# Kernel optimization log

Hardware: AMD Instinct MI355X
Metric: run time of the kernel (lower is better)

Reference implementation:

```python
import jax, jax.numpy as jnp
import numpy as np

K_PRESERVE = 256
NUM_NEW = 1
UNITS = 768
HEAD_DIM = 64
N_HEADS = UNITS // HEAD_DIM
HID = 768


def setup_inputs() -> dict:
    key = jax.random.key(0)
    ks = jax.random.split(key, 12)
    B, H, L, D = 32, 12, 512, HID
    s = 0.02
    return {
        "hidden_states": jax.random.normal(ks[0], (B, L, D), jnp.float32),
        "attention_mask": jnp.zeros((B, 1, 1, L), jnp.float32),
        "self_attention_scores": jax.random.normal(ks[1], (B, H, L, L), jnp.float32),
        "Wq": jax.random.normal(ks[2], (D, UNITS), jnp.float32) * s,
        "bq": jnp.zeros((UNITS,), jnp.float32),
        "Wk": jax.random.normal(ks[3], (D, UNITS), jnp.float32) * s,
        "bk": jnp.zeros((UNITS,), jnp.float32),
        "Wv": jax.random.normal(ks[4], (D, UNITS), jnp.float32) * s,
        "bv": jnp.zeros((UNITS,), jnp.float32),
        "Wo": jax.random.normal(ks[5], (UNITS, D), jnp.float32) * s,
        "bo": jnp.zeros((D,), jnp.float32),
    }


def _forward(hidden_states, attention_mask, self_attention_scores,
             Wq, bq, Wk, bk, Wv, bv, Wo, bo):
    B, L, D = hidden_states.shape
    # K after reserving the new token slot
    K = max(min(K_PRESERVE, L) - NUM_NEW, 1)

    am = attention_mask.reshape(B, L)                      # additive mask as [B,L]
    amf = (am > -10.0).astype(jnp.float32)
    elem = amf[:, :, None] * amf[:, None, :]               # [B,L,L]
    scores = self_attention_scores * elem[:, None, :, :]   # [B,H,L,L]

    imp = scores.mean(axis=1).mean(axis=1)                 # [B,L]
    imp = imp.at[:, 0].set(jnp.inf)                        # always keep CLS
    _, idx = jax.lax.top_k(imp, K)                         # [B,K]
    idx = jnp.sort(idx, axis=-1)                           # boolean-mask gather keeps order

    preserved = jnp.take_along_axis(hidden_states, idx[:, :, None], axis=1)  # [B,K,D]
    preserved_mask = jnp.take_along_axis(am, idx, axis=1).reshape(B, 1, 1, K)

    # sentence vector = softmax(mask) @ hidden
    att = jax.nn.softmax(am, axis=-1)                      # [B,L]
    sentences = jnp.einsum('bl,bld->bd', att, hidden_states)[:, None, :]  # [B,1,D]
    key_pad = am < -10.0                                    # [B,L] True = masked

    # small cross-attention producing one new token
    q = (sentences @ Wq + bq).reshape(B, 1, N_HEADS, HEAD_DIM)
    k = (hidden_states @ Wk + bk).reshape(B, L, N_HEADS, HEAD_DIM)
    v = (hidden_states @ Wv + bv).reshape(B, L, N_HEADS, HEAD_DIM)
    logits = jnp.einsum('bqhd,blhd->bhql', q, k) / np.sqrt(HEAD_DIM).astype(np.float32)
    logits = jnp.where(key_pad[:, None, None, :], -jnp.inf, logits)
    w = jax.nn.softmax(logits, axis=-1)                    # [B,H,1,L]
    ctx = jnp.einsum('bhql,blhd->bqhd', w, v).reshape(B, 1, UNITS)
    new_token = ctx @ Wo + bo                              # [B,1,D]

    final_token = jnp.concatenate([preserved, new_token], axis=1)         # [B,K+1,D]
    new_mask = jnp.zeros((B, 1, 1, 1), jnp.float32)
    final_mask = jnp.concatenate([preserved_mask, new_mask], axis=-1)     # [B,1,1,K+1]
    tome_size = jnp.ones((B, K + 1, 1), jnp.float32)
    return final_token, final_mask, tome_size


def reference(hidden_states, attention_mask, self_attention_scores,
              Wq, bq, Wk, bk, Wv, bv, Wo, bo):
    return _forward(hidden_states, attention_mask, self_attention_scores,
                    Wq, bq, Wk, bk, Wv, bv, Wo, bo)
```

## Files before the change

### kernel.cpp

```cpp
#include <hip/hip_runtime.h>
#include <cstdint>
#include <cstddef>

#define B 32
#define H 12
#define L 512
#define D 768
#define KSEL 255

#define OFF_IMP   0
#define MEMSET_BYTES 65536
#define OFF_SENT  65536
#define OFF_Y     163840
#define OFF_ATT   1343488
#define OFF_Q     1409024
#define OFF_A     1507328
#define OFF_CB    2686976
#define OFF_LG    2688512
#define OFF_SEL   3474944
#define OFF_CTX   3507584

__global__ __launch_bounds__(128) void k_imp(const float* __restrict__ sas,
                                             const float* __restrict__ am,
                                             float* __restrict__ imp) {
  const int b = blockIdx.x, h = blockIdx.y, ch = blockIdx.z;
  const int t = threadIdx.x;
  const float* base = sas + (((size_t)(b * H + h)) * L + (size_t)ch * 128) * L;
  const float* amb = am + b * L + ch * 128;
  float a0 = 0, a1 = 0, a2 = 0, a3 = 0;
#pragma unroll 8
  for (int l = 0; l < 128; ++l) {
    const float m = (amb[l] > -10.0f) ? 1.0f : 0.0f;
    const float4 v = reinterpret_cast<const float4*>(base + (size_t)l * L)[t];
    a0 += m * v.x;
    a1 += m * v.y;
    a2 += m * v.z;
    a3 += m * v.w;
  }
  float* ip = imp + b * L + t * 4;
  atomicAdd(ip + 0, a0);
  atomicAdd(ip + 1, a1);
  atomicAdd(ip + 2, a2);
  atomicAdd(ip + 3, a3);
}

__global__ __launch_bounds__(512) void k_prep(const float* __restrict__ am,
                                              const float* __restrict__ imp,
                                              float* __restrict__ att,
                                              int* __restrict__ sel,
                                              float* __restrict__ out_mask,
                                              float* __restrict__ out_tome,
                                              float* __restrict__ sent) {
  const int b = blockIdx.x, l = threadIdx.x;
  __shared__ float r1[8], r2[8];
  __shared__ float v[512];
  __shared__ int sc[512];
  sent[b * D + l] = 0.0f;
  if (l < D - 512) sent[b * D + 512 + l] = 0.0f;
  const float aml = am[b * L + l];
  float m = aml;
#pragma unroll
  for (int o = 32; o; o >>= 1) m = fmaxf(m, __shfl_down(m, o));
  if ((l & 63) == 0) r1[l >> 6] = m;
  __syncthreads();
  if (l == 0) {
    float mm = r1[0];
    for (int i = 1; i < 8; ++i) mm = fmaxf(mm, r1[i]);
    r1[0] = mm;
  }
  __syncthreads();
  const float M = r1[0];
  const float e = expf(aml - M);
  float s = e;
#pragma unroll
  for (int o = 32; o; o >>= 1) s += __shfl_down(s, o);
  if ((l & 63) == 0) r2[l >> 6] = s;
  __syncthreads();
  if (l == 0) {
    float ss = 0.f;
    for (int i = 0; i < 8; ++i) ss += r2[i];
    r2[0] = ss;
  }
  __syncthreads();
  att[b * L + l] = e / r2[0];
  float val;
  if (l == 0)
    val = INFINITY;
  else
    val = (aml > -10.0f) ? imp[b * L + l] : 0.0f;
  v[l] = val;
  __syncthreads();
  int r = 0;
  for (int t = 0; t < 512; ++t) {
    const float vt = v[t];
    r += (vt > val) || (vt == val && t < l);
  }
  const int f = (r < KSEL) ? 1 : 0;
  sc[l] = f;
  __syncthreads();
  for (int off = 1; off < 512; off <<= 1) {
    const int add = (l >= off) ? sc[l - off] : 0;
    __syncthreads();
    sc[l] += add;
    __syncthreads();
  }
  if (f) {
    const int pos = sc[l] - 1;
    sel[b * KSEL + pos] = l;
    out_mask[b * 256 + pos] = aml;
  }
  if (l == 0) out_mask[b * 256 + 255] = 0.0f;
  if (l < 256) out_tome[b * 256 + l] = 1.0f;
}

__global__ __launch_bounds__(256) void k_gather(const float* __restrict__ hs,
                                                const int* __restrict__ sel,
                                                float* __restrict__ out_tok) {
  const int row = blockIdx.x * 4 + (threadIdx.x >> 6);
  const int lane = threadIdx.x & 63;
  const int b = row / KSEL, p = row % KSEL;
  const int j = sel[row];
  const float4* src = reinterpret_cast<const float4*>(hs + ((size_t)b * L + j) * D);
  float4* dst = reinterpret_cast<float4*>(out_tok + ((size_t)b * 256 + p) * D);
#pragma unroll
  for (int i = 0; i < 3; ++i) dst[lane + 64 * i] = src[lane + 64 * i];
}

__global__ __launch_bounds__(768) void k_sent(const float* __restrict__ hs,
                                              const float* __restrict__ att,
                                              float* __restrict__ sent) {
  const int b = blockIdx.x, c = blockIdx.y, t = threadIdx.x;
  __shared__ float a[64];
  if (t < 64) a[t] = att[b * L + c * 64 + t];
  __syncthreads();
  const float* h0 = hs + ((size_t)b * L + c * 64) * D;
  float acc = 0.f;
  for (int l = 0; l < 64; ++l) acc += a[l] * h0[(size_t)l * D + t];
  atomicAdd(&sent[b * D + t], acc);
}

__global__ __launch_bounds__(512) void k_q(const float* __restrict__ sent,
                                           const float* __restrict__ Wq,
                                           const float* __restrict__ bq,
                                           const float* __restrict__ bk,
                                           float* __restrict__ qg,
                                           float* __restrict__ cbg) {
  const int h = blockIdx.x;
  const int b = blockIdx.y * 8 + (threadIdx.x >> 6);
  const int ul = threadIdx.x & 63;
  const int u = h * 64 + ul;
  const float* sb = sent + b * D;
  float a0 = 0.f, a1 = 0.f, a2 = 0.f, a3 = 0.f;
#pragma unroll 4
  for (int d = 0; d < D; d += 4) {
    a0 += sb[d + 0] * Wq[(size_t)(d + 0) * D + u];
    a1 += sb[d + 1] * Wq[(size_t)(d + 1) * D + u];
    a2 += sb[d + 2] * Wq[(size_t)(d + 2) * D + u];
    a3 += sb[d + 3] * Wq[(size_t)(d + 3) * D + u];
  }
  const float acc = bq[u] + ((a0 + a1) + (a2 + a3));
  qg[b * D + u] = acc;
  float v = bk[u] * acc;
#pragma unroll
  for (int o = 32; o; o >>= 1) v += __shfl_down(v, o);
  if (ul == 0) cbg[b * H + h] = v;
}

__global__ __launch_bounds__(1024) void k_A(const float* __restrict__ qg,
                                            const float* __restrict__ Wk,
                                            float* __restrict__ Ag) {
  const int h = blockIdx.x;
  const int dc = blockIdx.y;
  const int dl = threadIdx.x & 63;
  const int bl = threadIdx.x >> 6;
  __shared__ float tile[64][65];
  for (int i = threadIdx.x; i < 4096; i += 1024) {
    const int rr = i >> 6, cc = i & 63;
    tile[rr][cc] = Wk[(size_t)(dc * 64 + rr) * D + h * 64 + cc];
  }
  __syncthreads();
  const int d = dc * 64 + dl;
#pragma unroll
  for (int half = 0; half < 2; ++half) {
    const int b = half * 16 + bl;
    const float* qh = qg + b * D + h * 64;
    float acc = 0.f;
#pragma unroll
    for (int c = 0; c < 64; ++c) acc += tile[dl][c] * qh[c];
    Ag[((size_t)b * H + h) * D + d] = acc;
  }
}

__global__ __launch_bounds__(256) void k_logits(const float* __restrict__ hs,
                                                const float* __restrict__ Ag,
                                                const float* __restrict__ cbg,
                                                float* __restrict__ lg,
                                                float* __restrict__ y) {
  const int b = blockIdx.x, ch = blockIdx.y;
  if (ch == 0) {
    for (int i = threadIdx.x; i < H * D; i += 256) y[(size_t)b * H * D + i] = 0.0f;
  }
  __shared__ float A[H * D];
  for (int i = threadIdx.x; i < H * D; i += 256) A[i] = Ag[(size_t)b * H * D + i];
  __syncthreads();
  const int wave = threadIdx.x >> 6, lane = threadIdx.x & 63;
  const float* h0 = hs + (size_t)b * L * D;
  for (int li = 0; li < 8; ++li) {
    const int l = ch * 32 + li * 4 + wave;
    const float* xr = h0 + (size_t)l * D;
    float xv[12];
#pragma unroll
    for (int k = 0; k < 12; ++k) xv[k] = xr[lane + 64 * k];
#pragma unroll
    for (int h = 0; h < H; ++h) {
      float a = 0.f;
#pragma unroll
      for (int k = 0; k < 12; ++k) a += xv[k] * A[h * D + lane + 64 * k];
#pragma unroll
      for (int o = 32; o; o >>= 1) a += __shfl_down(a, o);
      if (lane == 0) lg[((size_t)b * H + h) * L + l] = (a + cbg[b * H + h]) * 0.125f;
    }
  }
}

__global__ __launch_bounds__(768) void k_ysoft(const float* __restrict__ hs,
                                               const float* __restrict__ lg,
                                               const float* __restrict__ am,
                                               float* __restrict__ y) {
  const int b = blockIdx.x, c = blockIdx.y, t = threadIdx.x;
  __shared__ float wl[H * L];
  __shared__ float Ms[H], Is[H];
  __shared__ float wn[H * 64];
  for (int i = t; i < H * L; i += 768) {
    const int l = i & (L - 1);
    const float aml = am[b * L + l];
    wl[i] = (aml < -10.0f) ? -INFINITY : lg[(size_t)b * H * L + i];
  }
  __syncthreads();
  {
    const int h = t >> 6, lane = t & 63;
    float m = -INFINITY;
#pragma unroll
    for (int k = 0; k < 8; ++k) m = fmaxf(m, wl[h * L + lane + 64 * k]);
#pragma unroll
    for (int o = 32; o; o >>= 1) m = fmaxf(m, __shfl_xor(m, o));
    float s = 0.f;
#pragma unroll
    for (int k = 0; k < 8; ++k) s += expf(wl[h * L + lane + 64 * k] - m);
#pragma unroll
    for (int o = 32; o; o >>= 1) s += __shfl_xor(s, o);
    if (lane == 0) { Ms[h] = m; Is[h] = 1.0f / s; }
  }
  __syncthreads();
  {
    const int h = t >> 6, l = t & 63;
    wn[t] = expf(wl[h * L + c * 64 + l] - Ms[h]) * Is[h];
  }
  __syncthreads();
  const float* h0 = hs + ((size_t)b * L + c * 64) * D;
  float acc[12];
#pragma unroll
  for (int h = 0; h < 12; ++h) acc[h] = 0.f;
  for (int l = 0; l < 64; ++l) {
    const float x = h0[(size_t)l * D + t];
#pragma unroll
    for (int h = 0; h < 12; ++h) acc[h] += wn[h * 64 + l] * x;
  }
#pragma unroll
  for (int h = 0; h < 12; ++h) atomicAdd(&y[((size_t)b * H + h) * D + t], acc[h]);
}

__global__ __launch_bounds__(512) void k_ctx(const float* __restrict__ y,
                                             const float* __restrict__ Wv,
                                             const float* __restrict__ bv,
                                             float* __restrict__ ctx) {
  const int h = blockIdx.x;
  const int b = blockIdx.y * 8 + (threadIdx.x >> 6);
  const int c = threadIdx.x & 63;
  const float* yb = y + ((size_t)b * H + h) * D;
  float a0 = 0.f, a1 = 0.f, a2 = 0.f, a3 = 0.f;
#pragma unroll 4
  for (int d = 0; d < D; d += 4) {
    a0 += yb[d + 0] * Wv[(size_t)(d + 0) * D + h * 64 + c];
    a1 += yb[d + 1] * Wv[(size_t)(d + 1) * D + h * 64 + c];
    a2 += yb[d + 2] * Wv[(size_t)(d + 2) * D + h * 64 + c];
    a3 += yb[d + 3] * Wv[(size_t)(d + 3) * D + h * 64 + c];
  }
  ctx[b * D + h * 64 + c] = bv[h * 64 + c] + ((a0 + a1) + (a2 + a3));
}

__global__ __launch_bounds__(512) void k_out(const float* __restrict__ ctx,
                                             const float* __restrict__ Wo,
                                             const float* __restrict__ bo,
                                             float* __restrict__ out_tok) {
  const int dc = blockIdx.x;
  const int b = blockIdx.y * 8 + (threadIdx.x >> 6);
  const int dl = threadIdx.x & 63;
  const int dd = dc * 64 + dl;
  const float* cb = ctx + b * D;
  float a0 = 0.f, a1 = 0.f, a2 = 0.f, a3 = 0.f;
#pragma unroll 4
  for (int u = 0; u < D; u += 4) {
    a0 += cb[u + 0] * Wo[(size_t)(u + 0) * D + dd];
    a1 += cb[u + 1] * Wo[(size_t)(u + 1) * D + dd];
    a2 += cb[u + 2] * Wo[(size_t)(u + 2) * D + dd];
    a3 += cb[u + 3] * Wo[(size_t)(u + 3) * D + dd];
  }
  out_tok[((size_t)b * 256 + 255) * D + dd] = bo[dd] + ((a0 + a1) + (a2 + a3));
}

extern "C" void kernel_launch(void* const* d_in, const int* in_sizes, int n_in,
                              void* d_out, int out_size, void* d_ws, size_t ws_size,
                              hipStream_t stream) {
  const float* hs = (const float*)d_in[0];
  const float* am = (const float*)d_in[1];
  const float* sas = (const float*)d_in[2];
  const float* Wq = (const float*)d_in[3];
  const float* bq = (const float*)d_in[4];
  const float* Wk = (const float*)d_in[5];
  const float* bk = (const float*)d_in[6];
  const float* Wv = (const float*)d_in[7];
  const float* bv = (const float*)d_in[8];
  const float* Wo = (const float*)d_in[9];
  const float* bo = (const float*)d_in[10];

  float* out_tok = (float*)d_out;
  float* out_mask = out_tok + (size_t)B * 256 * D;
  float* out_tome = out_mask + (size_t)B * 256;

  char* ws = (char*)d_ws;
  float* imp = (float*)(ws + OFF_IMP);
  float* sent = (float*)(ws + OFF_SENT);
  float* yg = (float*)(ws + OFF_Y);
  float* att = (float*)(ws + OFF_ATT);
  float* qg = (float*)(ws + OFF_Q);
  float* Ag = (float*)(ws + OFF_A);
  float* cbg = (float*)(ws + OFF_CB);
  float* lg = (float*)(ws + OFF_LG);
  int* sel = (int*)(ws + OFF_SEL);
  float* ctx = (float*)(ws + OFF_CTX);

  hipMemsetAsync(d_ws, 0, MEMSET_BYTES, stream);

  k_imp<<<dim3(B, H, 4), 128, 0, stream>>>(sas, am, imp);
  k_prep<<<B, 512, 0, stream>>>(am, imp, att, sel, out_mask, out_tome, sent);
  k_gather<<<(B * KSEL) / 4, 256, 0, stream>>>(hs, sel, out_tok);
  k_sent<<<dim3(B, 8), 768, 0, stream>>>(hs, att, sent);
  k_q<<<dim3(12, 4), 512, 0, stream>>>(sent, Wq, bq, bk, qg, cbg);
  k_A<<<dim3(12, 12), 1024, 0, stream>>>(qg, Wk, Ag);
  k_logits<<<dim3(B, 16), 256, 0, stream>>>(hs, Ag, cbg, lg, yg);
  k_ysoft<<<dim3(B, 8), 768, 0, stream>>>(hs, lg, am, yg);
  k_ctx<<<dim3(12, 4), 512, 0, stream>>>(yg, Wv, bv, ctx);
  k_out<<<dim3(12, 4), 512, 0, stream>>>(ctx, Wo, bo, out_tok);
}
```

Before: 773.7 us.

## Split importance reduction across fused kernels to overlap with attention branch

The big self-attention-score reduction is cut into three slices that run inside the first three kernels. Those kernels also carry the softmax/sentence/Q-projection work, so the independent attention-branch chain rides alongside the bandwidth-bound reduction instead of waiting behind it. The top-k selection and the Wk-projection share one launch, and the gather shares one with the logits. This cuts the launch count from 7 to 5 and fills idle CUs. Tiny branches now sit in large uniform 512-thread grids, so block-level syncs are shared across branches and the slices of imp rely on atomics finishing before k_f4 reads them.

```diff
diff --git a/kernel.cpp b/kernel.cpp
--- a/kernel.cpp
+++ b/kernel.cpp
@@ -10,216 +10,279 @@
 
 #define OFF_IMP   0
 #define MEMSET_BYTES 65536
-#define OFF_SENT  65536
-#define OFF_Y     163840
-#define OFF_ATT   1343488
-#define OFF_Q     1409024
-#define OFF_A     1507328
-#define OFF_CB    2686976
-#define OFF_LG    2688512
-#define OFF_SEL   3474944
+#define OFF_ATT   65536
+#define OFF_SENT  131072
+#define OFF_Q     229376
+#define OFF_CB    327680
+#define OFF_A     329216
+#define OFF_LG    1508864
+#define OFF_SEL   2295296
+#define OFF_Y     2327936
 #define OFF_CTX   3507584
 
-__global__ __launch_bounds__(128) void k_imp(const float* __restrict__ sas,
-                                             const float* __restrict__ am,
-                                             float* __restrict__ imp) {
-  const int b = blockIdx.x, h = blockIdx.y, ch = blockIdx.z;
-  const int t = threadIdx.x;
-  const float* base = sas + (((size_t)(b * H + h)) * L + (size_t)ch * 128) * L;
-  const float* amb = am + b * L + ch * 128;
+__device__ __forceinline__ void imp_slice(const float* __restrict__ sas,
+                                          const float* __restrict__ am,
+                                          float* __restrict__ imp,
+                                          int vb, int t, float4* red) {
+  const int b = vb / 48, r = vb % 48, h = r >> 2, ch = r & 3;
+  const int g = t >> 7, c = t & 127;
+  const int row0 = ch * 128 + g * 32;
+  const float* base = sas + (((size_t)(b * H + h)) * L + row0) * L;
+  const float* amb = am + b * L + row0;
   float a0 = 0, a1 = 0, a2 = 0, a3 = 0;
 #pragma unroll 8
-  for (int l = 0; l < 128; ++l) {
+  for (int l = 0; l < 32; ++l) {
     const float m = (amb[l] > -10.0f) ? 1.0f : 0.0f;
-    const float4 v = reinterpret_cast<const float4*>(base + (size_t)l * L)[t];
+    const float4 v = reinterpret_cast<const float4*>(base + (size_t)l * L)[c];
     a0 += m * v.x;
     a1 += m * v.y;
     a2 += m * v.z;
     a3 += m * v.w;
   }
-  float* ip = imp + b * L + t * 4;
-  atomicAdd(ip + 0, a0);
-  atomicAdd(ip + 1, a1);
-  atomicAdd(ip + 2, a2);
-  atomicAdd(ip + 3, a3);
-}
-
-__global__ __launch_bounds__(512) void k_prep(const float* __restrict__ am,
-                                              const float* __restrict__ imp,
-                                              float* __restrict__ att,
-                                              int* __restrict__ sel,
-                                              float* __restrict__ out_mask,
-                                              float* __restrict__ out_tome,
-                                              float* __restrict__ sent) {
-  const int b = blockIdx.x, l = threadIdx.x;
+  red[g * 128 + c] = make_float4(a0, a1, a2, a3);
+  __syncthreads();
+  if (g == 0) {
+    const float4 r0 = red[c], r1 = red[128 + c], r2 = red[256 + c], r3 = red[384 + c];
+    float* ip = imp + b * L + c * 4;
+    atomicAdd(ip + 0, r0.x + r1.x + r2.x + r3.x);
+    atomicAdd(ip + 1, r0.y + r1.y + r2.y + r3.y);
+    atomicAdd(ip + 2, r0.z + r1.z + r2.z + r3.z);
+    atomicAdd(ip + 3, r0.w + r1.w + r2.w + r3.w);
+  }
+}
+
+__global__ __launch_bounds__(512) void k_f1(const float* __restrict__ sas,
+                                            const float* __restrict__ am,
+                                            float* __restrict__ imp,
+                                            float* __restrict__ att,
+                                            float* __restrict__ sent) {
+  __shared__ float4 red[512];
   __shared__ float r1[8], r2[8];
+  const int bid = blockIdx.x, t = threadIdx.x;
+  imp_slice(sas, am, imp, bid, t, red);
+  if (bid < B) {
+    const int b = bid, l = t;
+    sent[b * D + l] = 0.0f;
+    if (l < D - 512) sent[b * D + 512 + l] = 0.0f;
+    const float aml = am[b * L + l];
+    float m = aml;
+#pragma unroll
+    for (int o = 32; o; o >>= 1) m = fmaxf(m, __shfl_down(m, o));
+    if ((l & 63) == 0) r1[l >> 6] = m;
+    __syncthreads();
+    if (l == 0) {
+      float mm = r1[0];
+      for (int i = 1; i < 8; ++i) mm = fmaxf(mm, r1[i]);
+      r1[0] = mm;
+    }
+    __syncthreads();
+    const float M = r1[0];
+    const float e = expf(aml - M);
+    float s = e;
+#pragma unroll
+    for (int o = 32; o; o >>= 1) s += __shfl_down(s, o);
+    if ((l & 63) == 0) r2[l >> 6] = s;
+    __syncthreads();
+    if (l == 0) {
+      float ss = 0.f;
+      for (int i = 0; i < 8; ++i) ss += r2[i];
+      r2[0] = ss;
+    }
+    __syncthreads();
+    att[b * L + l] = e / r2[0];
+  }
+}
+
+__global__ __launch_bounds__(512) void k_f2(const float* __restrict__ sas,
+                                            const float* __restrict__ am,
+                                            const float* __restrict__ hs,
+                                            const float* __restrict__ att,
+                                            float* __restrict__ imp,
+                                            float* __restrict__ sent) {
+  __shared__ float4 red[512];
+  __shared__ float a[64];
+  __shared__ float4 red2[8][192];
+  const int bid = blockIdx.x, t = threadIdx.x;
+  imp_slice(sas, am, imp, 512 + bid, t, red);
+  if (bid < 256) {
+    const int b = bid >> 3, c = bid & 7;
+    const int w = t >> 6, lane = t & 63;
+    if (t < 64) a[t] = att[b * L + c * 64 + t];
+    __syncthreads();
+    const float* h0 = hs + ((size_t)b * L + c * 64) * D;
+    float4 s0 = {0, 0, 0, 0}, s1 = {0, 0, 0, 0}, s2 = {0, 0, 0, 0};
+    for (int l = w; l < 64; l += 8) {
+      const float al = a[l];
+      const float4* row = reinterpret_cast<const float4*>(h0 + (size_t)l * D);
+      const float4 v0 = row[lane], v1 = row[lane + 64], v2 = row[lane + 128];
+      s0.x += al * v0.x; s0.y += al * v0.y; s0.z += al * v0.z; s0.w += al * v0.w;
+      s1.x += al * v1.x; s1.y += al * v1.y; s1.z += al * v1.z; s1.w += al * v1.w;
+      s2.x += al * v2.x; s2.y += al * v2.y; s2.z += al * v2.z; s2.w += al * v2.w;
+    }
+    red2[w][lane] = s0;
+    red2[w][lane + 64] = s1;
+    red2[w][lane + 128] = s2;
+    __syncthreads();
+    if (t < 192) {
+      float4 s = {0, 0, 0, 0};
+#pragma unroll
+      for (int ww = 0; ww < 8; ++ww) {
+        const float4 u = red2[ww][t];
+        s.x += u.x; s.y += u.y; s.z += u.z; s.w += u.w;
+      }
+      float* sp = sent + b * D + t * 4;
+      atomicAdd(sp + 0, s.x);
+      atomicAdd(sp + 1, s.y);
+      atomicAdd(sp + 2, s.z);
+      atomicAdd(sp + 3, s.w);
+    }
+  }
+}
+
+__global__ __launch_bounds__(512) void k_f3(const float* __restrict__ sas,
+                                            const float* __restrict__ am,
+                                            const float* __restrict__ sent,
+                                            const float* __restrict__ Wq,
+                                            const float* __restrict__ bq,
+                                            const float* __restrict__ bk,
+                                            float* __restrict__ imp,
+                                            float* __restrict__ qg,
+                                            float* __restrict__ cbg,
+                                            float* __restrict__ y) {
+  __shared__ float4 red[512];
+  const int bid = blockIdx.x, t = threadIdx.x;
+  imp_slice(sas, am, imp, 1024 + bid, t, red);
+  if (bid < 48) {
+    const int h = bid >> 2;
+    const int b = (bid & 3) * 8 + (t >> 6);
+    const int ul = t & 63;
+    const int u = h * 64 + ul;
+    const float* sb = sent + b * D;
+    float a0 = 0.f, a1 = 0.f, a2 = 0.f, a3 = 0.f;
+#pragma unroll 4
+    for (int d = 0; d < D; d += 4) {
+      a0 += sb[d + 0] * Wq[(size_t)(d + 0) * D + u];
+      a1 += sb[d + 1] * Wq[(size_t)(d + 1) * D + u];
+      a2 += sb[d + 2] * Wq[(size_t)(d + 2) * D + u];
+      a3 += sb[d + 3] * Wq[(size_t)(d + 3) * D + u];
+    }
+    const float acc = bq[u] + ((a0 + a1) + (a2 + a3));
+    qg[b * D + u] = acc;
+    float v = bk[u] * acc;
+#pragma unroll
+    for (int o = 32; o; o >>= 1) v += __shfl_down(v, o);
+    if (ul == 0) cbg[b * H + h] = v;
+  } else if (bid < 80) {
+    const int b = bid - 48;
+    for (int i = t; i < H * D; i += 512) y[(size_t)b * H * D + i] = 0.0f;
+  }
+}
+
+__global__ __launch_bounds__(512) void k_f4(const float* __restrict__ am,
+                                            const float* __restrict__ imp,
+                                            const float* __restrict__ qg,
+                                            const float* __restrict__ Wk,
+                                            int* __restrict__ sel,
+                                            float* __restrict__ out_mask,
+                                            float* __restrict__ out_tome,
+                                            float* __restrict__ Ag) {
+  const int bid = blockIdx.x, t = threadIdx.x;
   __shared__ float v[512];
   __shared__ int sc[512];
-  sent[b * D + l] = 0.0f;
-  if (l < D - 512) sent[b * D + 512 + l] = 0.0f;
-  const float aml = am[b * L + l];
-  float m = aml;
-#pragma unroll
-  for (int o = 32; o; o >>= 1) m = fmaxf(m, __shfl_down(m, o));
-  if ((l & 63) == 0) r1[l >> 6] = m;
-  __syncthreads();
-  if (l == 0) {
-    float mm = r1[0];
-    for (int i = 1; i < 8; ++i) mm = fmaxf(mm, r1[i]);
-    r1[0] = mm;
-  }
-  __syncthreads();
-  const float M = r1[0];
-  const float e = expf(aml - M);
-  float s = e;
-#pragma unroll
-  for (int o = 32; o; o >>= 1) s += __shfl_down(s, o);
-  if ((l & 63) == 0) r2[l >> 6] = s;
-  __syncthreads();
-  if (l == 0) {
-    float ss = 0.f;
-    for (int i = 0; i < 8; ++i) ss += r2[i];
-    r2[0] = ss;
-  }
-  __syncthreads();
-  att[b * L + l] = e / r2[0];
-  float val;
-  if (l == 0)
-    val = INFINITY;
-  else
-    val = (aml > -10.0f) ? imp[b * L + l] : 0.0f;
-  v[l] = val;
-  __syncthreads();
-  int r = 0;
-  for (int t = 0; t < 512; ++t) {
-    const float vt = v[t];
-    r += (vt > val) || (vt == val && t < l);
-  }
-  const int f = (r < KSEL) ? 1 : 0;
-  sc[l] = f;
-  __syncthreads();
-  for (int off = 1; off < 512; off <<= 1) {
-    const int add = (l >= off) ? sc[l - off] : 0;
-    __syncthreads();
-    sc[l] += add;
-    __syncthreads();
-  }
-  if (f) {
-    const int pos = sc[l] - 1;
-    sel[b * KSEL + pos] = l;
-    out_mask[b * 256 + pos] = aml;
-  }
-  if (l == 0) out_mask[b * 256 + 255] = 0.0f;
-  if (l < 256) out_tome[b * 256 + l] = 1.0f;
-}
-
-__global__ __launch_bounds__(256) void k_gather(const float* __restrict__ hs,
-                                                const int* __restrict__ sel,
-                                                float* __restrict__ out_tok) {
-  const int row = blockIdx.x * 4 + (threadIdx.x >> 6);
-  const int lane = threadIdx.x & 63;
-  const int b = row / KSEL, p = row % KSEL;
-  const int j = sel[row];
-  const float4* src = reinterpret_cast<const float4*>(hs + ((size_t)b * L + j) * D);
-  float4* dst = reinterpret_cast<float4*>(out_tok + ((size_t)b * 256 + p) * D);
-#pragma unroll
-  for (int i = 0; i < 3; ++i) dst[lane + 64 * i] = src[lane + 64 * i];
-}
-
-__global__ __launch_bounds__(768) void k_sent(const float* __restrict__ hs,
-                                              const float* __restrict__ att,
-                                              float* __restrict__ sent) {
-  const int b = blockIdx.x, c = blockIdx.y, t = threadIdx.x;
-  __shared__ float a[64];
-  if (t < 64) a[t] = att[b * L + c * 64 + t];
-  __syncthreads();
-  const float* h0 = hs + ((size_t)b * L + c * 64) * D;
-  float acc = 0.f;
-  for (int l = 0; l < 64; ++l) acc += a[l] * h0[(size_t)l * D + t];
-  atomicAdd(&sent[b * D + t], acc);
-}
-
-__global__ __launch_bounds__(512) void k_q(const float* __restrict__ sent,
-                                           const float* __restrict__ Wq,
-                                           const float* __restrict__ bq,
-                                           const float* __restrict__ bk,
-                                           float* __restrict__ qg,
-                                           float* __restrict__ cbg) {
-  const int h = blockIdx.x;
-  const int b = blockIdx.y * 8 + (threadIdx.x >> 6);
-  const int ul = threadIdx.x & 63;
-  const int u = h * 64 + ul;
-  const float* sb = sent + b * D;
-  float a0 = 0.f, a1 = 0.f, a2 = 0.f, a3 = 0.f;
-#pragma unroll 4
-  for (int d = 0; d < D; d += 4) {
-    a0 += sb[d + 0] * Wq[(size_t)(d + 0) * D + u];
-    a1 += sb[d + 1] * Wq[(size_t)(d + 1) * D + u];
-    a2 += sb[d + 2] * Wq[(size_t)(d + 2) * D + u];
-    a3 += sb[d + 3] * Wq[(size_t)(d + 3) * D + u];
-  }
-  const float acc = bq[u] + ((a0 + a1) + (a2 + a3));
-  qg[b * D + u] = acc;
-  float v = bk[u] * acc;
-#pragma unroll
-  for (int o = 32; o; o >>= 1) v += __shfl_down(v, o);
-  if (ul == 0) cbg[b * H + h] = v;
-}
-
-__global__ __launch_bounds__(1024) void k_A(const float* __restrict__ qg,
-                                            const float* __restrict__ Wk,
-                                            float* __restrict__ Ag) {
-  const int h = blockIdx.x;
-  const int dc = blockIdx.y;
-  const int dl = threadIdx.x & 63;
-  const int bl = threadIdx.x >> 6;
   __shared__ float tile[64][65];
-  for (int i = threadIdx.x; i < 4096; i += 1024) {
-    const int rr = i >> 6, cc = i & 63;
-    tile[rr][cc] = Wk[(size_t)(dc * 64 + rr) * D + h * 64 + cc];
-  }
-  __syncthreads();
-  const int d = dc * 64 + dl;
-#pragma unroll
-  for (int half = 0; half < 2; ++half) {
-    const int b = half * 16 + bl;
-    const float* qh = qg + b * D + h * 64;
-    float acc = 0.f;
-#pragma unroll
-    for (int c = 0; c < 64; ++c) acc += tile[dl][c] * qh[c];
-    Ag[((size_t)b * H + h) * D + d] = acc;
-  }
-}
-
-__global__ __launch_bounds__(256) void k_logits(const float* __restrict__ hs,
-                                                const float* __restrict__ Ag,
-                                                const float* __restrict__ cbg,
-                                                float* __restrict__ lg,
-                                                float* __restrict__ y) {
-  const int b = blockIdx.x, ch = blockIdx.y;
-  if (ch == 0) {
-    for (int i = threadIdx.x; i < H * D; i += 256) y[(size_t)b * H * D + i] = 0.0f;
-  }
+  if (bid < B) {
+    const int b = bid, l = t;
+    const float aml = am[b * L + l];
+    float val;
+    if (l == 0)
+      val = INFINITY;
+    else
+      val = (aml > -10.0f) ? imp[b * L + l] : 0.0f;
+    v[l] = val;
+    __syncthreads();
+    int r = 0;
+    for (int tt = 0; tt < 512; ++tt) {
+      const float vt = v[tt];
+      r += (vt > val) || (vt == val && tt < l);
+    }
+    const int f = (r < KSEL) ? 1 : 0;
+    sc[l] = f;
+    __syncthreads();
+    for (int off = 1; off < 512; off <<= 1) {
+      const int add = (l >= off) ? sc[l - off] : 0;
+      __syncthreads();
+      sc[l] += add;
+      __syncthreads();
+    }
+    if (f) {
+      const int pos = sc[l] - 1;
+      sel[b * KSEL + pos] = l;
+      out_mask[b * 256 + pos] = aml;
+    }
+    if (l == 0) out_mask[b * 256 + 255] = 0.0f;
+    if (l < 256) out_tome[b * 256 + l] = 1.0f;
+  } else {
+    const int vb = bid - B;
+    const int h = vb / 12, dc = vb % 12;
+    for (int i = t; i < 4096; i += 512) {
+      const int rr = i >> 6, cc = i & 63;
+      tile[rr][cc] = Wk[(size_t)(dc * 64 + rr) * D + h * 64 + cc];
+    }
+    __syncthreads();
+    const int dl = t & 63, bl = t >> 6;
+    const int d = dc * 64 + dl;
+#pragma unroll
+    for (int pass = 0; pass < 4; ++pass) {
+      const int b = pass * 8 + bl;
+      const float* qh = qg + b * D + h * 64;
+      float acc = 0.f;
+#pragma unroll
+      for (int c = 0; c < 64; ++c) acc += tile[dl][c] * qh[c];
+      Ag[((size_t)b * H + h) * D + d] = acc;
+    }
+  }
+}
+
+__global__ __launch_bounds__(256) void k_f5(const float* __restrict__ hs,
+                                            const float* __restrict__ Ag,
+                                            const float* __restrict__ cbg,
+                                            const int* __restrict__ sel,
+                                            float* __restrict__ lg,
+                                            float* __restrict__ out_tok) {
+  const int bid = blockIdx.x, t = threadIdx.x;
   __shared__ float A[H * D];
-  for (int i = threadIdx.x; i < H * D; i += 256) A[i] = Ag[(size_t)b * H * D + i];
-  __syncthreads();
-  const int wave = threadIdx.x >> 6, lane = threadIdx.x & 63;
-  const float* h0 = hs + (size_t)b * L * D;
-  for (int li = 0; li < 8; ++li) {
-    const int l = ch * 32 + li * 4 + wave;
-    const float* xr = h0 + (size_t)l * D;
-    float xv[12];
-#pragma unroll
-    for (int k = 0; k < 12; ++k) xv[k] = xr[lane + 64 * k];
-#pragma unroll
-    for (int h = 0; h < H; ++h) {
-      float a = 0.f;
-#pragma unroll
-      for (int k = 0; k < 12; ++k) a += xv[k] * A[h * D + lane + 64 * k];
-#pragma unroll
-      for (int o = 32; o; o >>= 1) a += __shfl_down(a, o);
-      if (lane == 0) lg[((size_t)b * H + h) * L + l] = (a + cbg[b * H + h]) * 0.125f;
-    }
+  if (bid < 512) {
+    const int b = bid >> 4, ch = bid & 15;
+    for (int i = t; i < H * D; i += 256) A[i] = Ag[(size_t)b * H * D + i];
+    __syncthreads();
+    const int wave = t >> 6, lane = t & 63;
+    const float* h0 = hs + (size_t)b * L * D;
+    for (int li = 0; li < 8; ++li) {
+      const int l = ch * 32 + li * 4 + wave;
+      const float* xr = h0 + (size_t)l * D;
+      float xv[12];
+#pragma unroll
+      for (int k = 0; k < 12; ++k) xv[k] = xr[lane + 64 * k];
+#pragma unroll
+      for (int h = 0; h < H; ++h) {
+        float a = 0.f;
+#pragma unroll
+        for (int k = 0; k < 12; ++k) a += xv[k] * A[h * D + lane + 64 * k];
+#pragma unroll
+        for (int o = 32; o; o >>= 1) a += __shfl_down(a, o);
+        if (lane == 0) lg[((size_t)b * H + h) * L + l] = (a + cbg[b * H + h]) * 0.125f;
+      }
+    }
+  } else {
+    const int vb = bid - 512;
+    const int row = vb * 4 + (t >> 6);
+    const int lane = t & 63;
+    const int b = row / KSEL, p = row % KSEL;
+    const int j = sel[row];
+    const float4* src = reinterpret_cast<const float4*>(hs + ((size_t)b * L + j) * D);
+    float4* dst = reinterpret_cast<float4*>(out_tok + ((size_t)b * 256 + p) * D);
+#pragma unroll
+    for (int i = 0; i < 3; ++i) dst[lane + 64 * i] = src[lane + 64 * i];
   }
 }
 
@@ -330,25 +393,23 @@
 
   char* ws = (char*)d_ws;
   float* imp = (float*)(ws + OFF_IMP);
+  float* att = (float*)(ws + OFF_ATT);
   float* sent = (float*)(ws + OFF_SENT);
-  float* yg = (float*)(ws + OFF_Y);
-  float* att = (float*)(ws + OFF_ATT);
   float* qg = (float*)(ws + OFF_Q);
+  float* cbg = (float*)(ws + OFF_CB);
   float* Ag = (float*)(ws + OFF_A);
-  float* cbg = (float*)(ws + OFF_CB);
   float* lg = (float*)(ws + OFF_LG);
   int* sel = (int*)(ws + OFF_SEL);
+  float* yg = (float*)(ws + OFF_Y);
   float* ctx = (float*)(ws + OFF_CTX);
 
   hipMemsetAsync(d_ws, 0, MEMSET_BYTES, stream);
 
-  k_imp<<<dim3(B, H, 4), 128, 0, stream>>>(sas, am, imp);
-  k_prep<<<B, 512, 0, stream>>>(am, imp, att, sel, out_mask, out_tome, sent);
-  k_gather<<<(B * KSEL) / 4, 256, 0, stream>>>(hs, sel, out_tok);
-  k_sent<<<dim3(B, 8), 768, 0, stream>>>(hs, att, sent);
-  k_q<<<dim3(12, 4), 512, 0, stream>>>(sent, Wq, bq, bk, qg, cbg);
-  k_A<<<dim3(12, 12), 1024, 0, stream>>>(qg, Wk, Ag);
-  k_logits<<<dim3(B, 16), 256, 0, stream>>>(hs, Ag, cbg, lg, yg);
+  k_f1<<<512, 512, 0, stream>>>(sas, am, imp, att, sent);
+  k_f2<<<512, 512, 0, stream>>>(sas, am, hs, att, imp, sent);
+  k_f3<<<512, 512, 0, stream>>>(sas, am, sent, Wq, bq, bk, imp, qg, cbg, yg);
+  k_f4<<<176, 512, 0, stream>>>(am, imp, qg, Wk, sel, out_mask, out_tome, Ag);
+  k_f5<<<2552, 256, 0, stream>>>(hs, Ag, cbg, sel, lg, out_tok);
   k_ysoft<<<dim3(B, 8), 768, 0, stream>>>(hs, lg, am, yg);
   k_ctx<<<dim3(12, 4), 512, 0, stream>>>(yg, Wv, bv, ctx);
   k_out<<<dim3(12, 4), 512, 0, stream>>>(ctx, Wo, bo, out_tok);
```

Measured after the change: 751.3 us. 1.03x faster.
